# Optimization experiments

Measured on AMD Instinct MI355X. Metric: run time of the kernel, lower is better.

The kernel has to match this reference:

```python
import jax, jax.numpy as jnp
import numpy as np

L, B, N, D, H = 18, 2, 1024, 256, 4
DH = D // H  # head_dim = 64
LAYER_TYPES = ("self", "cross") * 9
BN_EPS = 1e-5


def setup_inputs() -> dict:
    key = jax.random.key(0)
    ks = jax.random.split(key, 8)
    s = 0.03  # small init scale keeps 18 residual layers numerically tame
    w = lambda k, shape: jax.random.normal(k, shape, jnp.float32) * s
    return dict(
        descriptors=jax.random.normal(ks[0], (B, 2, N, D), jnp.float32),
        mask=jnp.ones((B, 2, N), jnp.int32),
        qw=w(ks[1], (L, D, D)), qb=jnp.zeros((L, D), jnp.float32),
        kw=w(ks[2], (L, D, D)), kb=jnp.zeros((L, D), jnp.float32),
        vw=w(ks[3], (L, D, D)), vb=jnp.zeros((L, D), jnp.float32),
        ow=w(ks[4], (L, D, D)), ob=jnp.zeros((L, D), jnp.float32),
        w1=w(ks[5], (L, 2 * D, 2 * D)), b1=jnp.zeros((L, 2 * D), jnp.float32),
        bn_g=jnp.ones((L, 2 * D), jnp.float32), bn_b=jnp.zeros((L, 2 * D), jnp.float32),
        w2=w(ks[6], (L, 2 * D, D)), b2=jnp.zeros((L, D), jnp.float32),
    )


def _attention(x, src, m, i, qw, qb, kw, kb, vw, vb, ow, ob):
    b, n, d = x.shape
    q = (x @ qw[i] + qb[i]).reshape(b, n, H, DH)
    k = (src @ kw[i] + kb[i]).reshape(b, -1, H, DH)
    v = (src @ vw[i] + vb[i]).reshape(b, -1, H, DH)
    scores = jnp.einsum("bnhd,bmhd->bhnm", q, k) / (DH ** 0.5)
    scores = jnp.where(m[:, None, None, :] == 0, jnp.float32(-1e9), scores)
    probs = jax.nn.softmax(scores, axis=-1)  # fp32, matches torch dtype=float32
    out = jnp.einsum("bhnm,bmhd->bnhd", probs, v).reshape(b, n, d)
    return out @ ow[i] + ob[i]


def _propagate(x, src, m, i, qw, qb, kw, kb, vw, vb, ow, ob, w1, b1, bn_g, bn_b, w2, b2):
    a = _attention(x, src, m, i, qw, qb, kw, kb, vw, vb, ow, ob)
    h = jnp.concatenate([x, a], axis=-1)        # [B, N, 2D]
    h = h @ w1[i] + b1[i]                       # [B, N, 2D]
    # BatchNorm1d (training mode): per-channel stats over batch and keypoint dims
    mean = h.mean(axis=(0, 1))
    var = ((h - mean) ** 2).mean(axis=(0, 1))   # biased variance, as torch BN uses
    h = (h - mean) / jnp.sqrt(var + BN_EPS) * bn_g[i] + bn_b[i]
    h = jax.nn.relu(h)
    return h @ w2[i] + b2[i]                    # [B, N, D]


def reference(descriptors, mask, qw, qb, kw, kb, vw, vb, ow, ob, w1, b1, bn_g, bn_b, w2, b2):
    d0, d1 = descriptors[:, 0], descriptors[:, 1]
    m0, m1 = mask[:, 0], mask[:, 1]
    params = (qw, qb, kw, kb, vw, vb, ow, ob, w1, b1, bn_g, bn_b, w2, b2)
    for i, lt in enumerate(LAYER_TYPES):
        if lt == "cross":
            s0, s1, sm0, sm1 = d1, d0, m1, m0
        else:  # self
            s0, s1, sm0, sm1 = d0, d1, m0, m1
        delta0 = _propagate(d0, s0, sm0, i, *params)
        delta1 = _propagate(d1, s1, sm1, i, *params)
        d0 = d0 + delta0
        d1 = d1 + delta1
    return jnp.stack([d0, d1], axis=1)
```

## Files before the change

kernel.cpp:

```cpp
#include <hip/hip_runtime.h>


typedef __attribute__((ext_vector_type(8))) short bf16x8;
typedef __attribute__((ext_vector_type(4))) short bf16x4;
typedef __attribute__((ext_vector_type(4))) float floatx4;

__device__ __forceinline__ short f2b(float f) {
  unsigned u = __builtin_bit_cast(unsigned, f);
  unsigned r = (u + 0x7FFFu + ((u >> 16) & 1u)) >> 16;
  return (short)r;
}
__device__ __forceinline__ unsigned pack2(float a, float b) {
  return (unsigned)(unsigned short)f2b(a) | ((unsigned)(unsigned short)f2b(b) << 16);
}
__device__ __forceinline__ void split2(float a, float b, unsigned& h, unsigned& l) {
  unsigned short ha = (unsigned short)f2b(a), hb = (unsigned short)f2b(b);
  float fa = __builtin_bit_cast(float, (unsigned)ha << 16);
  float fb = __builtin_bit_cast(float, (unsigned)hb << 16);
  h = (unsigned)ha | ((unsigned)hb << 16);
  l = pack2(a - fa, b - fb);
}

__device__ __forceinline__ void gl2lds16(const void* g, void* l) {
  __builtin_amdgcn_global_load_lds(
      (const __attribute__((address_space(1))) unsigned*)g,
      (__attribute__((address_space(3))) unsigned*)l, 16, 0, 0);
}

__device__ __forceinline__ floatx4 mfma16_bf16(bf16x4 a, bf16x4 b, floatx4 c) {
#if __has_builtin(__builtin_amdgcn_mfma_f32_16x16x16_bf16)
  return __builtin_amdgcn_mfma_f32_16x16x16_bf16(a, b, c, 0, 0, 0);
#elif __has_builtin(__builtin_amdgcn_mfma_f32_16x16x16bf16_1k)
  return __builtin_amdgcn_mfma_f32_16x16x16bf16_1k(a, b, c, 0, 0, 0);
#else
  asm volatile("v_mfma_f32_16x16x16_bf16 %0, %1, %2, %0" : "+v"(c) : "v"(a), "v"(b));
  return c;
#endif
}

#define BARW   asm volatile("s_barrier" ::: "memory")
#define WAITV8 asm volatile("s_waitcnt vmcnt(8)" ::: "memory")
#define WAITV5 asm volatile("s_waitcnt vmcnt(5)" ::: "memory")
#define WAITV4 asm volatile("s_waitcnt vmcnt(4)" ::: "memory")
#define WAITV0 asm volatile("s_waitcnt vmcnt(0)" ::: "memory")
#define LGKM0  asm volatile("s_waitcnt lgkmcnt(0)" ::: "memory")
#define PRIO1  __builtin_amdgcn_s_setprio(1)
#define PRIO0  __builtin_amdgcn_s_setprio(0)

#define GEMM_IDS                                        \
  const int tid = threadIdx.x;                          \
  const int lane = tid & 63, w = tid >> 6;              \
  const int wy = w >> 1, wx = w & 1;                    \
  const int quad = lane >> 4, l16 = lane & 15;          \
  const int lr = lane >> 3;                             \
  const int lcs = (((lane & 7) ^ lr) & 7) * 8;          \
  const floatx4 z4 = {0.f, 0.f, 0.f, 0.f};

__device__ __forceinline__ void mfma_step_sw(const short* As, const short* Bs,
                                             int wy, int wx, int quad, int l16,
                                             floatx4 acc[2][4]) {
#pragma unroll
  for (int kk = 0; kk < 2; ++kk) {
    const int sw = (((kk * 4 + quad) ^ (l16 & 7)) * 8);
    bf16x8 a0 = *(const bf16x8*)&As[(wy * 32 + l16) * 64 + sw];
    bf16x8 a1 = *(const bf16x8*)&As[(wy * 32 + 16 + l16) * 64 + sw];
    bf16x8 b[4];
#pragma unroll
    for (int ni = 0; ni < 4; ++ni)
      b[ni] = *(const bf16x8*)&Bs[(wx * 64 + ni * 16 + l16) * 64 + sw];
#pragma unroll
    for (int ni = 0; ni < 4; ++ni) {
      acc[0][ni] = __builtin_amdgcn_mfma_f32_16x16x32_bf16(a0, b[ni], acc[0][ni], 0, 0, 0);
      acc[1][ni] = __builtin_amdgcn_mfma_f32_16x16x32_bf16(a1, b[ni], acc[1][ni], 0, 0, 0);
    }
  }
}

__device__ __forceinline__ void mfma_step_sw32(const short* As, const short* Bs,
                                               int wy, int wx, int quad, int l16,
                                               floatx4 acc[4]) {
#pragma unroll
  for (int kk = 0; kk < 2; ++kk) {
    const int sw = (((kk * 4 + quad) ^ (l16 & 7)) * 8);
    bf16x8 a0 = *(const bf16x8*)&As[(wy * 16 + l16) * 64 + sw];
    bf16x8 b[4];
#pragma unroll
    for (int ni = 0; ni < 4; ++ni)
      b[ni] = *(const bf16x8*)&Bs[(wx * 64 + ni * 16 + l16) * 64 + sw];
#pragma unroll
    for (int ni = 0; ni < 4; ++ni)
      acc[ni] = __builtin_amdgcn_mfma_f32_16x16x32_bf16(a0, b[ni], acc[ni], 0, 0, 0);
  }
}

__device__ __forceinline__ void mfma_step_sw32x64(const short* As, const short* Bs,
                                                  int wy, int wx, int quad, int l16,
                                                  floatx4 acc[2]) {
#pragma unroll
  for (int kk = 0; kk < 2; ++kk) {
    const int sw = (((kk * 4 + quad) ^ (l16 & 7)) * 8);
    bf16x8 a0 = *(const bf16x8*)&As[(wy * 16 + l16) * 64 + sw];
    bf16x8 b[2];
#pragma unroll
    for (int ni = 0; ni < 2; ++ni)
      b[ni] = *(const bf16x8*)&Bs[(wx * 32 + ni * 16 + l16) * 64 + sw];
#pragma unroll
    for (int ni = 0; ni < 2; ++ni)
      acc[ni] = __builtin_amdgcn_mfma_f32_16x16x32_bf16(a0, b[ni], acc[ni], 0, 0, 0);
  }
}

__global__ __launch_bounds__(256) void wfuse(
    const float* __restrict__ ow, const float* __restrict__ w1,
    short* __restrict__ wbuf) {
  __shared__ short As_h[64 * 64], As_l[64 * 64];
  __shared__ short Bs_h[128 * 64], Bs_l[128 * 64];
  const int blk = blockIdx.x;
  const int layer = blk >> 4, sub = blk & 15;
  const int kp0 = (sub & 3) * 64, n0 = (sub >> 2) * 128;
  const float* A = ow + (size_t)layer * 65536;
  const float* Bw = w1 + (size_t)layer * 262144 + 256 * 512;
  short* w1t = wbuf + (size_t)layer * 655360 + 262144;
  GEMM_IDS;
  (void)lr; (void)lcs;
  floatx4 acc[2][4] = {{z4, z4, z4, z4}, {z4, z4, z4, z4}};
  const int ar = tid >> 2, aq = tid & 3;
  const int bn = tid & 127, bkh = tid >> 7;

  for (int s = 0; s < 4; ++s) {
    const int k0 = s * 64;
    const float* Ar = &A[(size_t)(kp0 + ar) * 256 + k0 + aq * 16];
    float4 f0 = *(const float4*)&Ar[0];
    float4 f1 = *(const float4*)&Ar[4];
    float4 f2 = *(const float4*)&Ar[8];
    float4 f3 = *(const float4*)&Ar[12];
    float bv[32];
#pragma unroll
    for (int kk2 = 0; kk2 < 32; ++kk2)
      bv[kk2] = Bw[(size_t)(k0 + bkh * 32 + kk2) * 512 + n0 + bn];

    __syncthreads();
    {
      uint4 hi, lo;
      split2(f0.x, f0.y, hi.x, lo.x);
      split2(f0.z, f0.w, hi.y, lo.y);
      split2(f1.x, f1.y, hi.z, lo.z);
      split2(f1.z, f1.w, hi.w, lo.w);
      int sl = ((aq * 2) ^ (ar & 7)) * 8;
      *(uint4*)&As_h[ar * 64 + sl] = hi;
      *(uint4*)&As_l[ar * 64 + sl] = lo;
      split2(f2.x, f2.y, hi.x, lo.x);
      split2(f2.z, f2.w, hi.y, lo.y);
      split2(f3.x, f3.y, hi.z, lo.z);
      split2(f3.z, f3.w, hi.w, lo.w);
      sl = ((aq * 2 + 1) ^ (ar & 7)) * 8;
      *(uint4*)&As_h[ar * 64 + sl] = hi;
      *(uint4*)&As_l[ar * 64 + sl] = lo;
    }
#pragma unroll
    for (int cc = 0; cc < 4; ++cc) {
      uint4 hi, lo;
      split2(bv[cc * 8 + 0], bv[cc * 8 + 1], hi.x, lo.x);
      split2(bv[cc * 8 + 2], bv[cc * 8 + 3], hi.y, lo.y);
      split2(bv[cc * 8 + 4], bv[cc * 8 + 5], hi.z, lo.z);
      split2(bv[cc * 8 + 6], bv[cc * 8 + 7], hi.w, lo.w);
      int sl = ((bkh * 4 + cc) ^ (bn & 7)) * 8;
      *(uint4*)&Bs_h[bn * 64 + sl] = hi;
      *(uint4*)&Bs_l[bn * 64 + sl] = lo;
    }
    __syncthreads();
    mfma_step_sw(As_h, Bs_h, wy, wx, quad, l16, acc);
    mfma_step_sw(As_h, Bs_l, wy, wx, quad, l16, acc);
    mfma_step_sw(As_l, Bs_h, wy, wx, quad, l16, acc);
  }
#pragma unroll
  for (int mi = 0; mi < 2; ++mi)
#pragma unroll
    for (int ni = 0; ni < 4; ++ni) {
      int col = n0 + wx * 64 + ni * 16 + l16;
      int row0 = kp0 + wy * 32 + mi * 16 + quad * 4;
      uint2 uu;
      uu.x = pack2(acc[mi][ni][0], acc[mi][ni][1]);
      uu.y = pack2(acc[mi][ni][2], acc[mi][ni][3]);
      *(uint2*)&w1t[(size_t)col * 512 + 256 + row0] = uu;
    }
}

__global__ __launch_bounds__(256) void wprep(
    const float* __restrict__ qw, const float* __restrict__ kw,
    const float* __restrict__ vw, const float* __restrict__ w1,
    const float* __restrict__ w2, const float* __restrict__ ob,
    const float* __restrict__ b1, short* __restrict__ wbuf,
    float* __restrict__ beff, const float* __restrict__ desc,
    float* __restrict__ xd, short* __restrict__ xb,
    float* __restrict__ psz) {
  __shared__ float SH[64 * 130];
  int blk = blockIdx.x;
  int t = threadIdx.x;
  if (blk < 1296) {
    int layer = blk / 72;
    int sub = blk % 72;
    const float* W; int Kd, Nd, k0, n0; size_t ooff;
    if (sub < 24) {
      int wsel = sub / 8; int tt = sub & 7;
      k0 = (tt >> 1) * 64; n0 = (tt & 1) * 128; Kd = 256; Nd = 256;
      W = (wsel == 0 ? qw : wsel == 1 ? kw : vw) + (size_t)layer * 65536;
      ooff = (size_t)wsel * 65536;
    } else if (sub < 56) {
      int tt = sub - 24; k0 = (tt >> 2) * 64; n0 = (tt & 3) * 128;
      Kd = 512; Nd = 512; W = w1 + (size_t)layer * 262144; ooff = 262144;
    } else {
      int tt = sub - 56; k0 = (tt >> 1) * 64; n0 = (tt & 1) * 128;
      Kd = 512; Nd = 256; W = w2 + (size_t)layer * 131072; ooff = 524288;
    }
    short* out = wbuf + (size_t)layer * 655360 + ooff;
    const int rr = t >> 4;
    const int c4 = (t & 15) * 4;
#pragma unroll
    for (int i = 0; i < 4; ++i)
#pragma unroll
      for (int hf = 0; hf < 2; ++hf) {
        float4 v = *(const float4*)&W[(size_t)(k0 + i * 16 + rr) * Nd + n0 + hf * 64 + c4];
        float* tp = &SH[(i * 16 + rr) * 130 + hf * 64 + c4];
        tp[0] = v.x; tp[1] = v.y; tp[2] = v.z; tp[3] = v.w;
      }
    __syncthreads();
    const int n = t >> 1;
    const int kh = (t & 1) * 32;
    float v[32];
#pragma unroll
    for (int kk = 0; kk < 32; ++kk)
      v[kk] = SH[(kh + kk) * 130 + n];
    unsigned u[16];
#pragma unroll
    for (int j2 = 0; j2 < 16; ++j2) u[j2] = pack2(v[2 * j2], v[2 * j2 + 1]);
    short* op = &out[(size_t)(n0 + n) * Kd + k0 + kh];
#pragma unroll
    for (int q4 = 0; q4 < 4; ++q4) {
      uint4 o; o.x = u[q4 * 4]; o.y = u[q4 * 4 + 1]; o.z = u[q4 * 4 + 2]; o.w = u[q4 * 4 + 3];
      *(uint4*)&op[q4 * 8] = o;
    }
  } else if (blk < 1440) {
    int bb = blk - 1296;
    int layer = bb >> 3;
    int n0 = (bb & 7) * 64;
    const float* obL = ob + (size_t)layer * 256;
    const float* w1L = w1 + (size_t)layer * 262144 + 256 * 512;
    int n = n0 + (t & 63);
    int part = t >> 6;
    float s = 0.f;
    for (int i = part * 64; i < part * 64 + 64; ++i)
      s += obL[i] * w1L[(size_t)i * 512 + n];
    SH[part * 64 + (t & 63)] = s;
    __syncthreads();
    if (t < 64) {
      float tot = SH[t] + SH[64 + t] + SH[128 + t] + SH[192 + t] +
                  b1[(size_t)layer * 512 + n0 + t];
      beff[(size_t)layer * 512 + n0 + t] = tot;
    }
  } else if (blk < 2464) {
    int idx = (blk - 1440) * 256 + t;
    int fi = idx << 2;
    int hi = (fi >> 19) & 1;
    int lo = (fi >> 18) & 1;
    int sj = (fi & ~(3 << 18)) | (lo << 19) | (hi << 18);
    float4 v = *(const float4*)&desc[sj];
    *(float4*)&xd[fi] = v;
    uint2 uu; uu.x = pack2(v.x, v.y); uu.y = pack2(v.z, v.w);
    *(uint2*)&xb[fi] = uu;
  } else {
    int idx = (blk - 2464) * 1024 + t * 4;
    float4 zz = {0.f, 0.f, 0.f, 0.f};
    *(float4*)&psz[idx] = zz;
  }
}

__global__ __launch_bounds__(256) void gemm_qkv(
    const short* __restrict__ xb, const short* __restrict__ wbufL,
    const float* __restrict__ qb_, const float* __restrict__ kb_,
    const float* __restrict__ vb_,
    short* __restrict__ q, short* __restrict__ kout, short* __restrict__ vT,
    int cross) {
  __shared__ short SM[2 * 2048 + 2 * 8192];
  short* As = SM;
  short* Bs = SM + 4096;
  const int rb = blockIdx.x * 32;
  const int cb = blockIdx.y * 128;
  const int seg = cb >> 8;
  const int cbl = cb & 255;
  int arb = rb;
  if (seg) arb = (rb & 2047) | ((((rb >> 11) ^ cross) & 1) << 11);
  const short* A = xb + (size_t)arb * 256;
  const short* Wt = wbufL + (size_t)seg * 65536 + (size_t)cbl * 256;
  const float* bias = (seg == 0 ? qb_ : seg == 1 ? kb_ : vb_) + cbl;
  GEMM_IDS;
  floatx4 acc[4] = {z4, z4, z4, z4};

#define QKV_STAGE(s, buf)                                                          \
  {                                                                                \
    int k0 = (s) * 64;                                                             \
    gl2lds16(&A[(size_t)(w * 8 + lr) * 256 + k0 + lcs], &As[(buf) * 2048 + (w * 8) * 64]); \
    _Pragma("unroll") for (int i = 0; i < 4; ++i)                                  \
      gl2lds16(&Wt[(size_t)(i * 32 + w * 8 + lr) * 256 + k0 + lcs],                \
               &Bs[(buf) * 8192 + (i * 32 + w * 8) * 64]);                         \
  }

  QKV_STAGE(0, 0);
  QKV_STAGE(1, 1);
  for (int s = 0; s < 4; ++s) {
    int buf = s & 1;
    if (s < 3) { WAITV5; } else { WAITV0; }
    BARW;
    PRIO1;
    mfma_step_sw32(&As[buf * 2048], &Bs[buf * 8192], wy, wx, quad, l16, acc);
    PRIO0;
    BARW;
    if (s < 2) QKV_STAGE(s + 2, buf);
  }

  if (seg < 2) {
    short* C = (seg == 0 ? q : kout) + (size_t)rb * 256 + cbl;
#pragma unroll
    for (int ni = 0; ni < 4; ++ni) {
      int col = wx * 64 + ni * 16 + l16;
      float bc = bias[col];
#pragma unroll
      for (int reg = 0; reg < 4; ++reg) {
        int row = wy * 16 + quad * 4 + reg;
        C[(size_t)row * 256 + col] = f2b(acc[ni][reg] + bc);
      }
    }
  } else {
    short* T = SM + 4096 + w * 1536;
    const int sb = rb >> 10;
    const int hh = (cbl >> 6) + wx;
    const int z = sb * 4 + hh;
#pragma unroll
    for (int ni = 0; ni < 4; ++ni) {
      int col = wx * 64 + ni * 16 + l16;
      float bc = bias[col];
#pragma unroll
      for (int reg = 0; reg < 4; ++reg)
        T[(ni * 16 + l16) * 24 + quad * 4 + reg] = f2b(acc[ni][reg] + bc);
    }
    short* dst = &vT[((size_t)z * 64 + lane) * 1024 + (rb & 1023) + wy * 16];
    *(uint4*)&dst[0] = *(const uint4*)&T[lane * 24 + 0];
    *(uint4*)&dst[8] = *(const uint4*)&T[lane * 24 + 8];
  }
#undef QKV_STAGE
}

__global__ __launch_bounds__(256) void attn_mfma(
    const short* __restrict__ q, const short* __restrict__ k,
    const short* __restrict__ vT, const int* __restrict__ mask,
    short* __restrict__ attnb, int cross) {
  __shared__ short Ks[2][2][4096];
  __shared__ short Vs[2][2][4096];
  __shared__ float Msk[1024];
  const int tid = threadIdx.x;
  const int lane = tid & 63, w = tid >> 6;
  const int wv = w & 1, wq = w >> 1;
  const int quad = lane >> 4, l16 = lane & 15;
  const int lr = lane >> 3;
  const int lcs = (((lane & 7) ^ lr) & 7) * 8;
  const int qt = blockIdx.x;
  const int z = blockIdx.y;
  const int sb = z >> 2, h = z & 3;
  const int s = sb >> 1, b = sb & 1;
  const int rowbase = sb * 1024;
  const int* mp = mask + (b * 2 + (s ^ cross)) * 1024;

  const int qrow = qt * 32 + wq * 16 + l16;
  bf16x8 qf[2];
#pragma unroll
  for (int kk = 0; kk < 2; ++kk)
    qf[kk] = *(const bf16x8*)&q[(size_t)(rowbase + qrow) * 256 + h * 64 + kk * 32 + quad * 8];

  {
    int4 mv = *(const int4*)&mp[tid * 4];
    Msk[tid * 4 + 0] = (mv.x == 0) ? -1.0e9f : 0.f;
    Msk[tid * 4 + 1] = (mv.y == 0) ? -1.0e9f : 0.f;
    Msk[tid * 4 + 2] = (mv.z == 0) ? -1.0e9f : 0.f;
    Msk[tid * 4 + 3] = (mv.w == 0) ? -1.0e9f : 0.f;
  }

  const floatx4 z4 = {0.f, 0.f, 0.f, 0.f};
  floatx4 o4[4] = {z4, z4, z4, z4};
  float mrun = -1e30f, lsum = 0.f;

#define ATT_STAGE(t, buf)                                                               \
  {                                                                                     \
    int key0s = wv * 512 + (t) * 64;                                                    \
    _Pragma("unroll") for (int j = 0; j < 4; ++j) {                                     \
      gl2lds16(&k[(size_t)(rowbase + key0s + j * 16 + wq * 8 + lr) * 256 + h * 64 + lcs], \
               &Ks[buf][wv][(j * 16 + wq * 8) * 64]);                                   \
      gl2lds16(&vT[((size_t)z * 64 + j * 16 + wq * 8 + lr) * 1024 + key0s + lcs],       \
               &Vs[buf][wv][(j * 16 + wq * 8) * 64]);                                   \
    }                                                                                   \
  }

  ATT_STAGE(0, 0);
  __syncthreads();
  for (int t = 0; t < 8; ++t) {
    int buf = t & 1;
    if (t < 7) { ATT_STAGE(t + 1, buf ^ 1); WAITV8; } else { WAITV0; }
    BARW;
    const int key0 = wv * 512 + t * 64;

    floatx4 sA[4] = {z4, z4, z4, z4};
    PRIO1;
#pragma unroll
    for (int kk = 0; kk < 2; ++kk) {
      const int sw = (((kk * 4 + quad) ^ (l16 & 7)) * 8);
#pragma unroll
      for (int mt = 0; mt < 4; ++mt) {
        bf16x8 kf = *(const bf16x8*)&Ks[buf][wv][(mt * 16 + l16) * 64 + sw];
        sA[mt] = __builtin_amdgcn_mfma_f32_16x16x32_bf16(kf, qf[kk], sA[mt], 0, 0, 0);
      }
    }
    PRIO0;
    float scv[4][4];
    float tmax = -1e30f;
#pragma unroll
    for (int mt = 0; mt < 4; ++mt) {
      float4 mk = *(const float4*)&Msk[key0 + mt * 16 + quad * 4];
      scv[mt][0] = sA[mt][0] * 0.125f + mk.x;
      scv[mt][1] = sA[mt][1] * 0.125f + mk.y;
      scv[mt][2] = sA[mt][2] * 0.125f + mk.z;
      scv[mt][3] = sA[mt][3] * 0.125f + mk.w;
#pragma unroll
      for (int reg = 0; reg < 4; ++reg) tmax = fmaxf(tmax, scv[mt][reg]);
    }
    tmax = fmaxf(tmax, __shfl_xor(tmax, 16));
    tmax = fmaxf(tmax, __shfl_xor(tmax, 32));
    float mnew = fmaxf(mrun, tmax);
    float corr = __expf(mrun - mnew);
    mrun = mnew;
    lsum *= corr;
#pragma unroll
    for (int dt = 0; dt < 4; ++dt)
#pragma unroll
      for (int reg = 0; reg < 4; ++reg) o4[dt][reg] *= corr;

    bf16x4 pb[4];
#pragma unroll
    for (int mt = 0; mt < 4; ++mt) {
      float e0 = __expf(scv[mt][0] - mnew);
      float e1 = __expf(scv[mt][1] - mnew);
      float e2 = __expf(scv[mt][2] - mnew);
      float e3 = __expf(scv[mt][3] - mnew);
      lsum += (e0 + e1) + (e2 + e3);
      union { bf16x4 v; uint2 u; } pu;
      pu.u.x = pack2(e0, e1); pu.u.y = pack2(e2, e3);
      pb[mt] = pu.v;
    }
    PRIO1;
#pragma unroll
    for (int mt = 0; mt < 4; ++mt) {
      const int c2 = mt * 2 + (quad >> 1);
      const int sub = (quad & 1) * 4;
#pragma unroll
      for (int dt = 0; dt < 4; ++dt) {
        bf16x4 vf = *(const bf16x4*)&Vs[buf][wv][(dt * 16 + l16) * 64 +
                                                 ((c2 ^ (l16 & 7)) * 8) + sub];
        o4[dt] = mfma16_bf16(vf, pb[mt], o4[dt]);
      }
    }
    PRIO0;
    LGKM0;
    BARW;
  }
  lsum += __shfl_xor(lsum, 16);
  lsum += __shfl_xor(lsum, 32);

  float* MG = (float*)&Ks[0][0][0];
  const int mo = (wq * 64 + lane) * 18;
  if (wv == 1) {
    MG[mo] = mrun;
    MG[mo + 1] = lsum;
#pragma unroll
    for (int dt = 0; dt < 4; ++dt)
#pragma unroll
      for (int reg = 0; reg < 4; ++reg) MG[mo + 2 + dt * 4 + reg] = o4[dt][reg];
  }
  __syncthreads();
  if (wv == 0) {
    float m2 = MG[mo], l2 = MG[mo + 1];
    float mm = fmaxf(mrun, m2);
    float ca = __expf(mrun - mm), cb2 = __expf(m2 - mm);
    float inv = 1.f / (ca * lsum + cb2 * l2);
    short* op = &attnb[(size_t)(rowbase + qrow) * 256 + h * 64 + quad * 4];
#pragma unroll
    for (int dt = 0; dt < 4; ++dt) {
      float v0 = (ca * o4[dt][0] + cb2 * MG[mo + 2 + dt * 4 + 0]) * inv;
      float v1 = (ca * o4[dt][1] + cb2 * MG[mo + 2 + dt * 4 + 1]) * inv;
      float v2 = (ca * o4[dt][2] + cb2 * MG[mo + 2 + dt * 4 + 2]) * inv;
      float v3 = (ca * o4[dt][3] + cb2 * MG[mo + 2 + dt * 4 + 3]) * inv;
      uint2 uu;
      uu.x = pack2(v0, v1);
      uu.y = pack2(v2, v3);
      *(uint2*)&op[dt * 16] = uu;
    }
  }
#undef ATT_STAGE
}

__global__ __launch_bounds__(256) void gemm_w1(
    const short* __restrict__ xb, const short* __restrict__ attnb,
    const short* __restrict__ w1t, const float* __restrict__ beff,
    float* __restrict__ hbuf, float* __restrict__ psumL, float* __restrict__ psqL) {
  __shared__ short SM[2 * 2048 + 2 * 8192];
  __shared__ float Ps[2][2][128];
  short* As = SM;
  short* Bs = SM + 4096;
  const int rb = blockIdx.x * 32, cb = blockIdx.y * 128;
  const int str = rb >> 11;
  GEMM_IDS;
  floatx4 acc[4] = {z4, z4, z4, z4};

#define W1_STAGE(s, buf)                                                            \
  {                                                                                 \
    int k0 = (s) * 64;                                                              \
    const short* Ap = ((s) < 4 ? xb : attnb) + (size_t)rb * 256;                    \
    int kb = k0 & 255;                                                              \
    gl2lds16(&Ap[(size_t)(w * 8 + lr) * 256 + kb + lcs], &As[(buf) * 2048 + (w * 8) * 64]); \
    _Pragma("unroll") for (int i = 0; i < 4; ++i)                                   \
      gl2lds16(&w1t[(size_t)(cb + i * 32 + w * 8 + lr) * 512 + k0 + lcs],           \
               &Bs[(buf) * 8192 + (i * 32 + w * 8) * 64]);                          \
  }

  W1_STAGE(0, 0);
  W1_STAGE(1, 1);
  for (int s = 0; s < 8; ++s) {
    int buf = s & 1;
    if (s < 7) { WAITV5; } else { WAITV0; }
    BARW;
    PRIO1;
    mfma_step_sw32(&As[buf * 2048], &Bs[buf * 8192], wy, wx, quad, l16, acc);
    PRIO0;
    BARW;
    if (s < 6) W1_STAGE(s + 2, buf);
  }
  float colsum[4], colsq[4];
#pragma unroll
  for (int ni = 0; ni < 4; ++ni) { colsum[ni] = 0.f; colsq[ni] = 0.f; }
#pragma unroll
  for (int ni = 0; ni < 4; ++ni) {
    int col = wx * 64 + ni * 16 + l16;
    float bc = beff[cb + col];
#pragma unroll
    for (int reg = 0; reg < 4; ++reg) {
      int row = rb + wy * 16 + quad * 4 + reg;
      float val = acc[ni][reg] + bc;
      hbuf[(size_t)row * 512 + cb + col] = val;
      colsum[ni] += val; colsq[ni] += val * val;
    }
  }
#pragma unroll
  for (int ni = 0; ni < 4; ++ni)
#pragma unroll
    for (int d = 16; d < 64; d <<= 1) {
      colsum[ni] += __shfl_xor(colsum[ni], d);
      colsq[ni]  += __shfl_xor(colsq[ni], d);
    }
  if (quad == 0) {
#pragma unroll
    for (int ni = 0; ni < 4; ++ni) {
      Ps[wy][0][wx * 64 + ni * 16 + l16] = colsum[ni];
      Ps[wy][1][wx * 64 + ni * 16 + l16] = colsq[ni];
    }
  }
  __syncthreads();
  if (tid < 128) {
    atomicAdd(&psumL[str * 512 + cb + tid], Ps[0][0][tid] + Ps[1][0][tid]);
    atomicAdd(&psqL [str * 512 + cb + tid], Ps[0][1][tid] + Ps[1][1][tid]);
  }
#undef W1_STAGE
}

__global__ __launch_bounds__(256) void gemm_w2(
    const float* __restrict__ hbuf, const short* __restrict__ w2t,
    const float* __restrict__ b2_, const float* __restrict__ psumL,
    const float* __restrict__ psqL, const float* __restrict__ g,
    const float* __restrict__ be, float* __restrict__ xd, short* __restrict__ xb,
    float* __restrict__ outp) {
  __shared__ short SM[2 * 2048 + 2 * 4096];
  __shared__ float s_scale[512], s_shift[512];
  short* As = SM;
  short* Bs = SM + 4096;
  const int rb = blockIdx.x * 32, cb = blockIdx.y * 64;
  const int str = rb >> 11;
  GEMM_IDS;
  floatx4 acc[2] = {z4, z4};
#pragma unroll
  for (int cc = 0; cc < 2; ++cc) {
    int c = tid + cc * 256;
    float sum = psumL[str * 512 + c];
    float sq  = psqL [str * 512 + c];
    float mean = sum * (1.f / 2048.f);
    float var = sq * (1.f / 2048.f) - mean * mean;
    float rstd = rsqrtf(var + 1e-5f);
    float gs = g[c] * rstd;
    s_scale[c] = gs;
    s_shift[c] = be[c] - mean * gs;
  }
  __syncthreads();

  const int p = tid & 7, ar = tid >> 3;
  float4 ra0, ra1;

#define W2_A_LOAD(s)                                                               \
  {                                                                                \
    int k0 = (s) * 64;                                                             \
    int cs = k0 + ((p ^ (ar & 7)) * 8);                                            \
    ra0 = *(const float4*)&hbuf[(size_t)(rb + ar) * 512 + cs];                     \
    ra1 = *(const float4*)&hbuf[(size_t)(rb + ar) * 512 + cs + 4];                 \
  }
#define W2_A_WRITE(s, buf)                                                         \
  {                                                                                \
    int k0 = (s) * 64;                                                             \
    int cs = k0 + ((p ^ (ar & 7)) * 8);                                            \
    float4 sc0 = *(const float4*)&s_scale[cs];                                     \
    float4 sc1 = *(const float4*)&s_scale[cs + 4];                                 \
    float4 sh0 = *(const float4*)&s_shift[cs];                                     \
    float4 sh1 = *(const float4*)&s_shift[cs + 4];                                 \
    uint4 pk;                                                                      \
    pk.x = pack2(fmaxf(ra0.x * sc0.x + sh0.x, 0.f), fmaxf(ra0.y * sc0.y + sh0.y, 0.f)); \
    pk.y = pack2(fmaxf(ra0.z * sc0.z + sh0.z, 0.f), fmaxf(ra0.w * sc0.w + sh0.w, 0.f)); \
    pk.z = pack2(fmaxf(ra1.x * sc1.x + sh1.x, 0.f), fmaxf(ra1.y * sc1.y + sh1.y, 0.f)); \
    pk.w = pack2(fmaxf(ra1.z * sc1.z + sh1.z, 0.f), fmaxf(ra1.w * sc1.w + sh1.w, 0.f)); \
    *(uint4*)&As[(buf) * 2048 + ar * 64 + p * 8] = pk;                             \
  }
#define W2_STAGE_B(s, buf)                                                         \
  {                                                                                \
    int k0 = (s) * 64;                                                             \
    _Pragma("unroll") for (int i = 0; i < 2; ++i)                                  \
      gl2lds16(&w2t[(size_t)(cb + i * 32 + w * 8 + lr) * 512 + k0 + lcs],          \
               &Bs[(buf) * 4096 + (i * 32 + w * 8) * 64]);                         \
  }

  W2_A_LOAD(0);
  W2_STAGE_B(0, 0);
  W2_A_WRITE(0, 0);
  LGKM0;
  for (int s = 0; s < 8; ++s) {
    int buf = s & 1;
    if (s < 7) { W2_A_LOAD(s + 1); W2_STAGE_B(s + 1, buf ^ 1); WAITV4; } else { WAITV0; }
    BARW;
    PRIO1;
    mfma_step_sw32x64(&As[buf * 2048], &Bs[buf * 4096], wy, wx, quad, l16, acc);
    PRIO0;
    if (s < 7) W2_A_WRITE(s + 1, buf ^ 1);
    LGKM0;
    BARW;
  }
#pragma unroll
  for (int ni = 0; ni < 2; ++ni) {
    int col = cb + wx * 32 + ni * 16 + l16;
    float bc = b2_[col];
#pragma unroll
    for (int reg = 0; reg < 4; ++reg) {
      int row = rb + wy * 16 + quad * 4 + reg;
      float r = xd[(size_t)row * 256 + col] + acc[ni][reg] + bc;
      xd[(size_t)row * 256 + col] = r;
      xb[(size_t)row * 256 + col] = f2b(r);
      if (outp) {
        int ss = row >> 11, bb = (row >> 10) & 1, n = row & 1023;
        outp[(size_t)((bb * 2 + ss) * 1024 + n) * 256 + col] = r;
      }
    }
  }
#undef W2_A_LOAD
#undef W2_A_WRITE
#undef W2_STAGE_B
}

extern "C" void kernel_launch(void* const* d_in, const int* in_sizes, int n_in,
                              void* d_out, int out_size, void* d_ws, size_t ws_size,
                              hipStream_t stream) {
  (void)in_sizes; (void)n_in; (void)out_size; (void)ws_size;
  const float* desc = (const float*)d_in[0];
  const int*   mask = (const int*)d_in[1];
  const float* qw = (const float*)d_in[2];
  const float* qb = (const float*)d_in[3];
  const float* kw = (const float*)d_in[4];
  const float* kb = (const float*)d_in[5];
  const float* vw = (const float*)d_in[6];
  const float* vb = (const float*)d_in[7];
  const float* ow = (const float*)d_in[8];
  const float* ob = (const float*)d_in[9];
  const float* w1 = (const float*)d_in[10];
  const float* b1 = (const float*)d_in[11];
  const float* bn_g = (const float*)d_in[12];
  const float* bn_b = (const float*)d_in[13];
  const float* w2 = (const float*)d_in[14];
  const float* b2 = (const float*)d_in[15];
  float* out = (float*)d_out;

  char* base = (char*)d_ws;
  float* xd    = (float*)(base);
  float* hbuf  = (float*)(base + (4u << 20));
  short* xb    = (short*)(base + (12u << 20));
  short* qb16  = (short*)(base + (14u << 20));
  short* kb16  = (short*)(base + (16u << 20));
  short* vTb   = (short*)(base + (18u << 20));
  short* attnb = (short*)(base + (20u << 20));
  float* psum  = (float*)(base + (22u << 20));
  float* psq   = psum + 18 * 1024;
  float* beff  = psq + 18 * 1024;
  short* wbuf  = (short*)(base + (24u << 20));

  wprep<<<2500, 256, 0, stream>>>(qw, kw, vw, w1, w2, ob, b1,
                                  wbuf, beff, desc, xd, xb, psum);
  wfuse<<<288, 256, 0, stream>>>(ow, w1, wbuf);

  for (int i = 0; i < 18; ++i) {
    int cross = i & 1;
    short* wb = wbuf + (size_t)i * 655360;

    gemm_qkv<<<dim3(128, 6), 256, 0, stream>>>(
        xb, wb, qb + (size_t)i * 256, kb + (size_t)i * 256, vb + (size_t)i * 256,
        qb16, kb16, vTb, cross);
    attn_mfma<<<dim3(32, 16), 256, 0, stream>>>(qb16, kb16, vTb, mask, attnb, cross);
    gemm_w1<<<dim3(128, 4), 256, 0, stream>>>(xb, attnb, wb + 262144,
                                              beff + (size_t)i * 512,
                                              hbuf, psum + (size_t)i * 1024,
                                              psq + (size_t)i * 1024);
    gemm_w2<<<dim3(128, 4), 256, 0, stream>>>(hbuf, wb + 524288,
                                              b2 + (size_t)i * 256,
                                              psum + (size_t)i * 1024,
                                              psq + (size_t)i * 1024,
                                              bn_g + (size_t)i * 512,
                                              bn_b + (size_t)i * 512, xd, xb,
                                              (i == 17) ? out : nullptr);
  }
}
```

Before: 946.3 us.

## Replace double-buffered K pipeline with bulk-load-then-compute in projection GEMMs

The three projection GEMMs (QKV, W1, W2) drop their two-stage double-buffered K loop. Each now issues all loads for a 256-wide K chunk into a larger LDS buffer, waits once, and runs the MFMA steps back to back. This cuts per-step barriers and waitcnt stalls, and launch bounds now ask for 2–3 resident blocks per CU so other blocks can hide the load latency. The cost is more LDS per block, no load/compute overlap inside a block, and the LDS reuse for the V transpose and the partial BN sums needs extra barriers.

Measured after the change: 933.0 us. No clear change (-1.4%).

```diff
diff --git a/kernel.cpp b/kernel.cpp
--- a/kernel.cpp
+++ b/kernel.cpp
@@ -40,8 +40,6 @@
 
 #define BARW   asm volatile("s_barrier" ::: "memory")
 #define WAITV8 asm volatile("s_waitcnt vmcnt(8)" ::: "memory")
-#define WAITV5 asm volatile("s_waitcnt vmcnt(5)" ::: "memory")
-#define WAITV4 asm volatile("s_waitcnt vmcnt(4)" ::: "memory")
 #define WAITV0 asm volatile("s_waitcnt vmcnt(0)" ::: "memory")
 #define LGKM0  asm volatile("s_waitcnt lgkmcnt(0)" ::: "memory")
 #define PRIO1  __builtin_amdgcn_s_setprio(1)
@@ -275,15 +273,15 @@
   }
 }
 
-__global__ __launch_bounds__(256) void gemm_qkv(
+__global__ __launch_bounds__(256, 2) void gemm_qkv(
     const short* __restrict__ xb, const short* __restrict__ wbufL,
     const float* __restrict__ qb_, const float* __restrict__ kb_,
     const float* __restrict__ vb_,
     short* __restrict__ q, short* __restrict__ kout, short* __restrict__ vT,
     int cross) {
-  __shared__ short SM[2 * 2048 + 2 * 8192];
+  __shared__ short SM[40960];
   short* As = SM;
-  short* Bs = SM + 4096;
+  short* Bs = SM + 8192;
   const int rb = blockIdx.x * 32;
   const int cb = blockIdx.y * 128;
   const int seg = cb >> 8;
@@ -296,27 +294,20 @@
   GEMM_IDS;
   floatx4 acc[4] = {z4, z4, z4, z4};
 
-#define QKV_STAGE(s, buf)                                                          \
-  {                                                                                \
-    int k0 = (s) * 64;                                                             \
-    gl2lds16(&A[(size_t)(w * 8 + lr) * 256 + k0 + lcs], &As[(buf) * 2048 + (w * 8) * 64]); \
-    _Pragma("unroll") for (int i = 0; i < 4; ++i)                                  \
-      gl2lds16(&Wt[(size_t)(i * 32 + w * 8 + lr) * 256 + k0 + lcs],                \
-               &Bs[(buf) * 8192 + (i * 32 + w * 8) * 64]);                         \
-  }
-
-  QKV_STAGE(0, 0);
-  QKV_STAGE(1, 1);
+#pragma unroll
   for (int s = 0; s < 4; ++s) {
-    int buf = s & 1;
-    if (s < 3) { WAITV5; } else { WAITV0; }
-    BARW;
-    PRIO1;
-    mfma_step_sw32(&As[buf * 2048], &Bs[buf * 8192], wy, wx, quad, l16, acc);
-    PRIO0;
-    BARW;
-    if (s < 2) QKV_STAGE(s + 2, buf);
-  }
+    const int k0 = s * 64;
+    gl2lds16(&A[(size_t)(w * 8 + lr) * 256 + k0 + lcs], &As[s * 2048 + (w * 8) * 64]);
+#pragma unroll
+    for (int i = 0; i < 4; ++i)
+      gl2lds16(&Wt[(size_t)(i * 32 + w * 8 + lr) * 256 + k0 + lcs],
+               &Bs[s * 8192 + (i * 32 + w * 8) * 64]);
+  }
+  WAITV0;
+  BARW;
+#pragma unroll
+  for (int s = 0; s < 4; ++s)
+    mfma_step_sw32(&As[s * 2048], &Bs[s * 8192], wy, wx, quad, l16, acc);
 
   if (seg < 2) {
     short* C = (seg == 0 ? q : kout) + (size_t)rb * 256 + cbl;
@@ -331,7 +322,8 @@
       }
     }
   } else {
-    short* T = SM + 4096 + w * 1536;
+    BARW;
+    short* T = SM + w * 1536;
     const int sb = rb >> 10;
     const int hh = (cbl >> 6) + wx;
     const int z = sb * 4 + hh;
@@ -347,7 +339,6 @@
     *(uint4*)&dst[0] = *(const uint4*)&T[lane * 24 + 0];
     *(uint4*)&dst[8] = *(const uint4*)&T[lane * 24 + 8];
   }
-#undef QKV_STAGE
 }
 
 __global__ __launch_bounds__(256) void attn_mfma(
@@ -505,42 +496,39 @@
 #undef ATT_STAGE
 }
 
-__global__ __launch_bounds__(256) void gemm_w1(
+__global__ __launch_bounds__(256, 2) void gemm_w1(
     const short* __restrict__ xb, const short* __restrict__ attnb,
     const short* __restrict__ w1t, const float* __restrict__ beff,
     float* __restrict__ hbuf, float* __restrict__ psumL, float* __restrict__ psqL) {
-  __shared__ short SM[2 * 2048 + 2 * 8192];
-  __shared__ float Ps[2][2][128];
+  __shared__ short SM[40960];
   short* As = SM;
-  short* Bs = SM + 4096;
+  short* Bs = SM + 8192;
   const int rb = blockIdx.x * 32, cb = blockIdx.y * 128;
   const int str = rb >> 11;
   GEMM_IDS;
   floatx4 acc[4] = {z4, z4, z4, z4};
 
-#define W1_STAGE(s, buf)                                                            \
-  {                                                                                 \
-    int k0 = (s) * 64;                                                              \
-    const short* Ap = ((s) < 4 ? xb : attnb) + (size_t)rb * 256;                    \
-    int kb = k0 & 255;                                                              \
-    gl2lds16(&Ap[(size_t)(w * 8 + lr) * 256 + kb + lcs], &As[(buf) * 2048 + (w * 8) * 64]); \
-    _Pragma("unroll") for (int i = 0; i < 4; ++i)                                   \
-      gl2lds16(&w1t[(size_t)(cb + i * 32 + w * 8 + lr) * 512 + k0 + lcs],           \
-               &Bs[(buf) * 8192 + (i * 32 + w * 8) * 64]);                          \
-  }
-
-  W1_STAGE(0, 0);
-  W1_STAGE(1, 1);
-  for (int s = 0; s < 8; ++s) {
-    int buf = s & 1;
-    if (s < 7) { WAITV5; } else { WAITV0; }
+#pragma unroll
+  for (int h = 0; h < 2; ++h) {
+    if (h) BARW;
+    const short* Ap = (h == 0 ? xb : attnb) + (size_t)rb * 256;
+#pragma unroll
+    for (int st = 0; st < 4; ++st) {
+      const int k0 = h * 256 + st * 64;
+      gl2lds16(&Ap[(size_t)(w * 8 + lr) * 256 + st * 64 + lcs],
+               &As[st * 2048 + (w * 8) * 64]);
+#pragma unroll
+      for (int i = 0; i < 4; ++i)
+        gl2lds16(&w1t[(size_t)(cb + i * 32 + w * 8 + lr) * 512 + k0 + lcs],
+                 &Bs[st * 8192 + (i * 32 + w * 8) * 64]);
+    }
+    WAITV0;
     BARW;
-    PRIO1;
-    mfma_step_sw32(&As[buf * 2048], &Bs[buf * 8192], wy, wx, quad, l16, acc);
-    PRIO0;
-    BARW;
-    if (s < 6) W1_STAGE(s + 2, buf);
-  }
+#pragma unroll
+    for (int st = 0; st < 4; ++st)
+      mfma_step_sw32(&As[st * 2048], &Bs[st * 8192], wy, wx, quad, l16, acc);
+  }
+
   float colsum[4], colsq[4];
 #pragma unroll
   for (int ni = 0; ni < 4; ++ni) { colsum[ni] = 0.f; colsq[ni] = 0.f; }
@@ -563,6 +551,8 @@
       colsum[ni] += __shfl_xor(colsum[ni], d);
       colsq[ni]  += __shfl_xor(colsq[ni], d);
     }
+  __syncthreads();
+  float (*Ps)[2][128] = (float(*)[2][128])SM;
   if (quad == 0) {
 #pragma unroll
     for (int ni = 0; ni < 4; ++ni) {
@@ -575,19 +565,18 @@
     atomicAdd(&psumL[str * 512 + cb + tid], Ps[0][0][tid] + Ps[1][0][tid]);
     atomicAdd(&psqL [str * 512 + cb + tid], Ps[0][1][tid] + Ps[1][1][tid]);
   }
-#undef W1_STAGE
-}
-
-__global__ __launch_bounds__(256) void gemm_w2(
+}
+
+__global__ __launch_bounds__(256, 3) void gemm_w2(
     const float* __restrict__ hbuf, const short* __restrict__ w2t,
     const float* __restrict__ b2_, const float* __restrict__ psumL,
     const float* __restrict__ psqL, const float* __restrict__ g,
     const float* __restrict__ be, float* __restrict__ xd, short* __restrict__ xb,
     float* __restrict__ outp) {
-  __shared__ short SM[2 * 2048 + 2 * 4096];
+  __shared__ short SM[24576];
   __shared__ float s_scale[512], s_shift[512];
   short* As = SM;
-  short* Bs = SM + 4096;
+  short* Bs = SM + 8192;
   const int rb = blockIdx.x * 32, cb = blockIdx.y * 64;
   const int str = rb >> 11;
   GEMM_IDS;
@@ -607,53 +596,42 @@
   __syncthreads();
 
   const int p = tid & 7, ar = tid >> 3;
-  float4 ra0, ra1;
-
-#define W2_A_LOAD(s)                                                               \
-  {                                                                                \
-    int k0 = (s) * 64;                                                             \
-    int cs = k0 + ((p ^ (ar & 7)) * 8);                                            \
-    ra0 = *(const float4*)&hbuf[(size_t)(rb + ar) * 512 + cs];                     \
-    ra1 = *(const float4*)&hbuf[(size_t)(rb + ar) * 512 + cs + 4];                 \
-  }
-#define W2_A_WRITE(s, buf)                                                         \
-  {                                                                                \
-    int k0 = (s) * 64;                                                             \
-    int cs = k0 + ((p ^ (ar & 7)) * 8);                                            \
-    float4 sc0 = *(const float4*)&s_scale[cs];                                     \
-    float4 sc1 = *(const float4*)&s_scale[cs + 4];                                 \
-    float4 sh0 = *(const float4*)&s_shift[cs];                                     \
-    float4 sh1 = *(const float4*)&s_shift[cs + 4];                                 \
-    uint4 pk;                                                                      \
-    pk.x = pack2(fmaxf(ra0.x * sc0.x + sh0.x, 0.f), fmaxf(ra0.y * sc0.y + sh0.y, 0.f)); \
-    pk.y = pack2(fmaxf(ra0.z * sc0.z + sh0.z, 0.f), fmaxf(ra0.w * sc0.w + sh0.w, 0.f)); \
-    pk.z = pack2(fmaxf(ra1.x * sc1.x + sh1.x, 0.f), fmaxf(ra1.y * sc1.y + sh1.y, 0.f)); \
-    pk.w = pack2(fmaxf(ra1.z * sc1.z + sh1.z, 0.f), fmaxf(ra1.w * sc1.w + sh1.w, 0.f)); \
-    *(uint4*)&As[(buf) * 2048 + ar * 64 + p * 8] = pk;                             \
-  }
-#define W2_STAGE_B(s, buf)                                                         \
-  {                                                                                \
-    int k0 = (s) * 64;                                                             \
-    _Pragma("unroll") for (int i = 0; i < 2; ++i)                                  \
-      gl2lds16(&w2t[(size_t)(cb + i * 32 + w * 8 + lr) * 512 + k0 + lcs],          \
-               &Bs[(buf) * 4096 + (i * 32 + w * 8) * 64]);                         \
-  }
-
-  W2_A_LOAD(0);
-  W2_STAGE_B(0, 0);
-  W2_A_WRITE(0, 0);
-  LGKM0;
-  for (int s = 0; s < 8; ++s) {
-    int buf = s & 1;
-    if (s < 7) { W2_A_LOAD(s + 1); W2_STAGE_B(s + 1, buf ^ 1); WAITV4; } else { WAITV0; }
-    BARW;
-    PRIO1;
-    mfma_step_sw32x64(&As[buf * 2048], &Bs[buf * 4096], wy, wx, quad, l16, acc);
-    PRIO0;
-    if (s < 7) W2_A_WRITE(s + 1, buf ^ 1);
+
+#pragma unroll
+  for (int h = 0; h < 2; ++h) {
+    if (h) BARW;
+#pragma unroll
+    for (int st = 0; st < 4; ++st) {
+      const int k0 = h * 256 + st * 64;
+#pragma unroll
+      for (int i = 0; i < 2; ++i)
+        gl2lds16(&w2t[(size_t)(cb + i * 32 + w * 8 + lr) * 512 + k0 + lcs],
+                 &Bs[st * 4096 + (i * 32 + w * 8) * 64]);
+    }
+#pragma unroll
+    for (int st = 0; st < 4; ++st) {
+      const int cs = h * 256 + st * 64 + ((p ^ (ar & 7)) * 8);
+      float4 h0 = *(const float4*)&hbuf[(size_t)(rb + ar) * 512 + cs];
+      float4 h1 = *(const float4*)&hbuf[(size_t)(rb + ar) * 512 + cs + 4];
+      float4 sc0 = *(const float4*)&s_scale[cs];
+      float4 sc1 = *(const float4*)&s_scale[cs + 4];
+      float4 sh0 = *(const float4*)&s_shift[cs];
+      float4 sh1 = *(const float4*)&s_shift[cs + 4];
+      uint4 pk;
+      pk.x = pack2(fmaxf(h0.x * sc0.x + sh0.x, 0.f), fmaxf(h0.y * sc0.y + sh0.y, 0.f));
+      pk.y = pack2(fmaxf(h0.z * sc0.z + sh0.z, 0.f), fmaxf(h0.w * sc0.w + sh0.w, 0.f));
+      pk.z = pack2(fmaxf(h1.x * sc1.x + sh1.x, 0.f), fmaxf(h1.y * sc1.y + sh1.y, 0.f));
+      pk.w = pack2(fmaxf(h1.z * sc1.z + sh1.z, 0.f), fmaxf(h1.w * sc1.w + sh1.w, 0.f));
+      *(uint4*)&As[st * 2048 + ar * 64 + p * 8] = pk;
+    }
+    WAITV0;
     LGKM0;
     BARW;
-  }
+#pragma unroll
+    for (int st = 0; st < 4; ++st)
+      mfma_step_sw32x64(&As[st * 2048], &Bs[st * 4096], wy, wx, quad, l16, acc);
+  }
+
 #pragma unroll
   for (int ni = 0; ni < 2; ++ni) {
     int col = cb + wx * 32 + ni * 16 + l16;
@@ -670,9 +648,6 @@
       }
     }
   }
-#undef W2_A_LOAD
-#undef W2_A_WRITE
-#undef W2_STAGE_B
 }
 
 extern "C" void kernel_launch(void* const* d_in, const int* in_sizes, int n_in,
```
